# Kernel optimization log

Measured on AMD Instinct MI355X. Metric: run time of the kernel, lower is better.

## Reference

```python
import jax, jax.numpy as jnp
import numpy as np

EPS_BN = 1e-5
EPS_COS = 1e-8

N, F_IN, HID, OUT, S, NNZ = 50000, 1024, 256, 280, 5000, 800000


def setup_inputs() -> dict:
    key = jax.random.key(0)
    ks = jax.random.split(key, 20)
    inp = {}
    inp["x"] = jax.random.normal(ks[0], (N, F_IN), jnp.float32)
    inp["y"] = jax.random.normal(ks[1], (S, OUT), jnp.float32)
    inp["adj_rows"] = jax.random.randint(ks[2], (NNZ,), 0, N, jnp.int32)
    inp["adj_cols"] = jax.random.randint(ks[3], (NNZ,), 0, N, jnp.int32)
    inp["adj_vals"] = jax.random.uniform(ks[4], (NNZ,), jnp.float32)
    inp["agg_rows"] = jax.random.randint(ks[5], (N,), 0, S, jnp.int32)
    inp["agg_vals"] = jax.random.uniform(ks[6], (N,), jnp.float32)
    inp["perm"] = jax.random.permutation(ks[7], N).astype(jnp.int32)
    # parameters (kaiming-ish scale)
    def lin(k, fi, fo):
        k1, k2 = jax.random.split(k)
        w = jax.random.normal(k1, (fi, fo), jnp.float32) / np.sqrt(fi)
        b = jax.random.normal(k2, (fo,), jnp.float32) * 0.01
        return w, b
    inp["mlp_W"], inp["mlp_b"] = lin(ks[8], F_IN, HID)
    inp["bn_gamma"] = jnp.ones((HID,), jnp.float32)
    inp["bn_beta"] = jnp.zeros((HID,), jnp.float32)
    inp["hg_W1"], inp["hg_b1"] = lin(ks[9], HID, HID)
    inp["hg_W2"], inp["hg_b2"] = lin(ks[10], HID, HID)
    inp["hg_prelu"] = jnp.float32(0.25)
    inp["pred_W"], inp["pred_b"] = lin(ks[11], HID, OUT)
    inp["dgi_W"], inp["dgi_b"] = lin(ks[12], HID, OUT)
    inp["dgi_prelu"] = jnp.float32(0.25)
    return inp


def _spmm(rows, cols, vals, M, n_out):
    # sparse(H) @ M : gather source rows, scale by edge value, scatter-add to dest
    return jax.ops.segment_sum(vals[:, None] * M[cols], rows, num_segments=n_out)


def _prelu(t, a):
    return jnp.where(t >= 0, t, a * t)


def _leaky(t, s):
    return jnp.where(t >= 0, t, s * t)


def reference(x, y, adj_rows, adj_cols, adj_vals, agg_rows, agg_vals, perm,
              mlp_W, mlp_b, bn_gamma, bn_beta, hg_W1, hg_b1, hg_W2, hg_b2,
              hg_prelu, pred_W, pred_b, dgi_W, dgi_b, dgi_prelu):
    n = x.shape[0]
    s = y.shape[0]
    # mlp: Linear -> LeakyReLU(0.1) -> BatchNorm1d (batch stats, training mode)
    h0 = _leaky(x @ mlp_W + mlp_b, 0.1)
    mu = jnp.mean(h0, axis=0)
    var = jnp.mean((h0 - mu) ** 2, axis=0)  # biased, as torch BN training
    h0 = bn_gamma * (h0 - mu) * jax.lax.rsqrt(var + EPS_BN) + bn_beta
    # HGNN, num_layers=2 (dropout = identity in eval)
    t = _spmm(adj_rows, adj_cols, adj_vals, h0 @ hg_W1 + hg_b1, n)
    t = _prelu(t, hg_prelu)
    t = _spmm(adj_rows, adj_cols, adj_vals, t @ hg_W2 + hg_b2, n)
    h = _leaky(t, 0.01)
    x_prime = _leaky(h @ pred_W + pred_b, 0.01)
    # Xenium: loss = MSE(agg_mtx @ x_prime, y); agg_mtx has one nnz per cell
    agg = jax.ops.segment_sum(agg_vals[:, None] * x_prime, agg_rows, num_segments=s)
    loss = jnp.mean((agg - y) ** 2)
    # DGI (1-layer HGNN with PReLU)
    h1 = _prelu(_spmm(adj_rows, adj_cols, adj_vals, h0 @ dgi_W + dgi_b, n), dgi_prelu)
    c = jnp.mean(h1, axis=0)  # (OUT,)
    h2 = _prelu(_spmm(adj_rows, adj_cols, adj_vals, h0[perm] @ dgi_W + dgi_b, n), dgi_prelu)
    c_norm = jnp.linalg.norm(c)
    def cos(hm):
        return (hm @ c) / jnp.maximum(jnp.linalg.norm(hm, axis=1) * c_norm, EPS_COS)
    loss = loss + jnp.mean(1.0 - cos(h1)) + jnp.mean(jnp.maximum(cos(h2), 0.0))
    return (loss, x_prime)
```

## Files before the change

### kernel.cpp

```cpp
#include <hip/hip_runtime.h>
#include <hip/hip_bf16.h>

#define DEVI __device__ __forceinline__

typedef __attribute__((ext_vector_type(8))) short short8;
typedef __attribute__((ext_vector_type(4))) float float4v;

DEVI float bf2f(__hip_bfloat16 v) { return __bfloat162float(v); }
DEVI float ldbs(const ushort* p, size_t i) { return bf2f(((const __hip_bfloat16*)p)[i]); }
DEVI ushort f2bs(float v) {
    __hip_bfloat16 h = __float2bfloat16(v);
    return *(ushort*)&h;
}
DEVI float bfs2f(short s) {
    ushort u = (ushort)s;
    return bf2f(*(__hip_bfloat16*)&u);
}

DEVI float ldin(const void* p, size_t i, int isf32) {
    return isf32 ? ((const float*)p)[i] : bf2f(((const __hip_bfloat16*)p)[i]);
}
DEVI void stio(void* p, size_t i, float v, int isf32) {
    if (isf32) ((float*)p)[i] = v;
    else ((ushort*)p)[i] = f2bs(v);
}

template <int ACT>
DEVI float act_fn(float v, float alpha) {
    if (ACT == 1) return v >= 0.f ? v : 0.1f * v;
    if (ACT == 2) return v >= 0.f ? v : 0.01f * v;
    if (ACT == 3) return v >= 0.f ? v : alpha * v;
    return v;
}

DEVI float waveRed(float v) {
#pragma unroll
    for (int o = 32; o > 0; o >>= 1) v += __shfl_down(v, o);
    return v;
}

DEVI float blockRed(float v) {
    __shared__ float sm[16];
    int lane = threadIdx.x & 63, w = threadIdx.x >> 6;
    v = waveRed(v);
    if (lane == 0) sm[w] = v;
    __syncthreads();
    if (w == 0) {
        int nw = (blockDim.x + 63) >> 6;
        v = (lane < nw) ? sm[lane] : 0.f;
        v = waveRed(v);
    }
    return v;
}

__global__ void probe_k(const void* __restrict__ x, int* __restrict__ flag) {
    __shared__ int sfails;
    int t = threadIdx.x;
    if (t == 0) sfails = 0;
    __syncthreads();
    const __hip_bfloat16* xb = (const __hip_bfloat16*)x;
    int my = 0;
    for (int i = t; i < 4096; i += 256) {
        float v = bf2f(xb[i]);
        float a = fabsf(v);
        if (!(a <= 64.f) || (v != 0.f && a < 1e-6f)) my++;
    }
    atomicAdd(&sfails, my);
    __syncthreads();
    if (t == 0) flag[0] = (sfails > 409) ? 1 : 0;
}

struct Cvt5 {
    const void* src[5];
    ushort* dst[5];
    int K[5];
    int N[5];
};
__global__ void cvt_all_k(Cvt5 d, const int* __restrict__ flagp) {
    int f32 = flagp[0];
    int seg = blockIdx.y;
    int idx = blockIdx.x * blockDim.x + threadIdx.x;
    int K = d.K[seg], Nc = d.N[seg];
    int total = K * Nc;
    if (idx < total) {
        int k = idx / Nc, n = idx % Nc;
        d.dst[seg][(size_t)n * K + k] = f2bs(ldin(d.src[seg], idx, f32));
    }
}

#define TP 40
template <int AMODE, int ACT, int OMODE>
__global__ __launch_bounds__(256) void mgemm_k(
    const void* __restrict__ A, const ushort* __restrict__ Bt,
    const void* __restrict__ bias, void* __restrict__ outp, ushort* __restrict__ outp2,
    const int* __restrict__ flagp, int M, int K, int Nc, int LDo) {
    __shared__ short As[128 * TP];
    __shared__ short Bs[128 * TP];
    const int f32 = flagp[0];
    const int tid = threadIdx.x;
    const int lane = tid & 63;
    const int l15 = lane & 15;
    const int quad = lane >> 4;
    const int wid = tid >> 6;
    const int mW = (wid >> 1) * 64;
    const int nW = (wid & 1) * 64;
    const int mBase = blockIdx.y * 128;
    const int nBase = blockIdx.x * 128;

    float4v acc[4][4];
#pragma unroll
    for (int i = 0; i < 4; i++)
#pragma unroll
        for (int j = 0; j < 4; j++) acc[i][j] = (float4v){0.f, 0.f, 0.f, 0.f};

    short8 sa[2], sb[2];
    float4v fa[2][2];

    auto issue_tile = [&](int k0) {
#pragma unroll
        for (int i = 0; i < 2; i++) {
            int chunk = i * 256 + tid;
            int row = chunk >> 2;
            int c = chunk & 3;
            int gr = mBase + row;
            int gn = nBase + row;
            size_t geA = (size_t)gr * K + k0 + c * 8;
            if (AMODE == 0 && f32) {
                if (gr < M) {
                    const float* af = (const float*)A + geA;
                    fa[i][0] = *(const float4v*)af;
                    fa[i][1] = *(const float4v*)(af + 4);
                } else {
                    fa[i][0] = (float4v){0.f, 0.f, 0.f, 0.f};
                    fa[i][1] = (float4v){0.f, 0.f, 0.f, 0.f};
                }
            } else {
                sa[i] = (gr < M) ? *(const short8*)((const ushort*)A + geA)
                                 : (short8){0, 0, 0, 0, 0, 0, 0, 0};
            }
            sb[i] = (gn < Nc) ? *(const short8*)(Bt + (size_t)gn * K + k0 + c * 8)
                              : (short8){0, 0, 0, 0, 0, 0, 0, 0};
        }
    };

    auto commit_tile = [&]() {
#pragma unroll
        for (int i = 0; i < 2; i++) {
            int chunk = i * 256 + tid;
            int row = chunk >> 2;
            int c = chunk & 3;
            short8 va;
            if (AMODE == 0 && f32) {
#pragma unroll
                for (int j = 0; j < 4; j++) va[j] = (short)f2bs(fa[i][0][j]);
#pragma unroll
                for (int j = 0; j < 4; j++) va[4 + j] = (short)f2bs(fa[i][1][j]);
            } else {
                va = sa[i];
            }
            *(short8*)&As[row * TP + c * 8] = va;
            *(short8*)&Bs[row * TP + c * 8] = sb[i];
        }
    };

    const int nk = K >> 5;
    issue_tile(0);
    for (int t = 0; t < nk; ++t) {
        __syncthreads();
        commit_tile();
        if (t + 1 < nk) issue_tile((t + 1) << 5);
        __syncthreads();

        short8 af[4], bf[4];
#pragma unroll
        for (int i = 0; i < 4; i++)
            af[i] = *(const short8*)&As[(mW + i * 16 + l15) * TP + quad * 8];
#pragma unroll
        for (int j = 0; j < 4; j++)
            bf[j] = *(const short8*)&Bs[(nW + j * 16 + l15) * TP + quad * 8];
#pragma unroll
        for (int i = 0; i < 4; i++)
#pragma unroll
            for (int j = 0; j < 4; j++)
                acc[i][j] =
                    __builtin_amdgcn_mfma_f32_16x16x32_bf16(af[i], bf[j], acc[i][j], 0, 0, 0);
    }

#pragma unroll
    for (int i = 0; i < 4; i++) {
#pragma unroll
        for (int j = 0; j < 4; j++) {
            int gcn = nBase + nW + j * 16 + l15;
            if (gcn >= Nc) continue;
            float bv = ldin(bias, gcn, f32);
#pragma unroll
            for (int r = 0; r < 4; r++) {
                int grm = mBase + mW + i * 16 + quad * 4 + r;
                if (grm >= M) continue;
                float v = act_fn<ACT>(acc[i][j][r] + bv, 0.f);
                if (OMODE == 1) {
                    stio(outp, 1 + (size_t)grm * Nc + gcn, v, f32);
                    outp2[(size_t)grm * LDo + gcn] = f2bs(v);
                } else {
                    ((ushort*)outp)[(size_t)grm * LDo + gcn] = f2bs(v);
                }
            }
        }
    }
}

__global__ void count_k(const int* __restrict__ rows, int* __restrict__ counts, int nnz) {
    int i = blockIdx.x * blockDim.x + threadIdx.x;
    if (i < nnz) atomicAdd(&counts[rows[i]], 1);
}

__global__ __launch_bounds__(1024) void scan_local_k(const int* __restrict__ counts,
                                                     int* __restrict__ offs,
                                                     int* __restrict__ bsums, int n) {
    __shared__ int sm[1024];
    int t = threadIdx.x;
    int g = blockIdx.x * 1024 + t;
    int v = (g < n) ? counts[g] : 0;
    sm[t] = v;
    __syncthreads();
    for (int d = 1; d < 1024; d <<= 1) {
        int add = (t >= d) ? sm[t - d] : 0;
        __syncthreads();
        sm[t] += add;
        __syncthreads();
    }
    if (g < n) offs[g] = sm[t] - v;
    if (t == 1023) bsums[blockIdx.x] = sm[t];
}

__global__ void scan_bsums_k(int* bsums, int nb) {
    if (threadIdx.x == 0 && blockIdx.x == 0) {
        int acc = 0;
        for (int i = 0; i < nb; i++) {
            int v = bsums[i];
            bsums[i] = acc;
            acc += v;
        }
    }
}

__global__ void scan_add_k(int* __restrict__ offs, const int* __restrict__ bsums, int n, int nnz) {
    int g = blockIdx.x * blockDim.x + threadIdx.x;
    if (g < n) offs[g] += bsums[g >> 10];
    if (g == 0) offs[n] = nnz;
}

__global__ void fill_k(const int* __restrict__ rows, const int* __restrict__ cols,
                       const void* __restrict__ vals, const int* __restrict__ perm,
                       const int* __restrict__ offs, int* __restrict__ cursor,
                       int* __restrict__ cols_s, int* __restrict__ colsp_s,
                       float* __restrict__ vals_s, const int* __restrict__ flagp, int nnz) {
    int e = blockIdx.x * blockDim.x + threadIdx.x;
    if (e < nnz) {
        int r = rows[e];
        int pos = offs[r] + atomicAdd(&cursor[r], 1);
        int c = cols[e];
        cols_s[pos] = c;
        colsp_s[pos] = perm[c];
        vals_s[pos] = ldin(vals, e, flagp[0]);
    }
}

__global__ void fill_s_k(const int* __restrict__ rows, const void* __restrict__ vals,
                         const int* __restrict__ offs, int* __restrict__ cursor,
                         int* __restrict__ idx_s, float* __restrict__ val_s,
                         const int* __restrict__ flagp, int n) {
    int e = blockIdx.x * blockDim.x + threadIdx.x;
    if (e < n) {
        int r = rows[e];
        int pos = offs[r] + atomicAdd(&cursor[r], 1);
        idx_s[pos] = e;
        val_s[pos] = ldin(vals, e, flagp[0]);
    }
}

template <int ACT, bool DUAL>
__global__ __launch_bounds__(256) void spmmv_k(
    const int* __restrict__ offs, const int* __restrict__ cols_s,
    const int* __restrict__ colsp_s, const float* __restrict__ vals_s,
    const void* __restrict__ alpha_p, const int* __restrict__ flagp,
    const ushort* __restrict__ Min, ushort* __restrict__ out1, ushort* __restrict__ out2,
    int Nrow, int F, int LDin) {
    int row = blockIdx.x * 4 + (threadIdx.x >> 6);
    if (row >= Nrow) return;
    int lane = threadIdx.x & 63;
    int half = lane >> 5, l5 = lane & 31;
    int FC = F >> 3;
    bool has1 = (l5 + 32) < FC;
    float alpha = (ACT == 3) ? ldin(alpha_p, 0, flagp[0]) : 0.f;
    int s = offs[row], e = offs[row + 1];
    float a0[8] = {}, a1[8] = {}, b0[8] = {}, b1[8] = {};

    constexpr int DEPTH = DUAL ? 2 : 4;
    int i = s + half;
    for (; i + 2 * (DEPTH - 1) < e; i += 2 * DEPTH) {
        int c[DEPTH];
        float v[DEPTH];
        int cp[DEPTH];
#pragma unroll
        for (int u = 0; u < DEPTH; u++) {
            c[u] = cols_s[i + 2 * u];
            v[u] = vals_s[i + 2 * u];
        }
        if (DUAL) {
#pragma unroll
            for (int u = 0; u < DEPTH; u++) cp[u] = colsp_s[i + 2 * u];
        }
        short8 h0v[DEPTH], h1v[DEPTH], g0v[DEPTH], g1v[DEPTH];
#pragma unroll
        for (int u = 0; u < DEPTH; u++) {
            const ushort* src = Min + (size_t)c[u] * LDin;
            h0v[u] = *(const short8*)(src + l5 * 8);
            if (has1) h1v[u] = *(const short8*)(src + (l5 + 32) * 8);
            if (DUAL) {
                const ushort* srcp = Min + (size_t)cp[u] * LDin;
                g0v[u] = *(const short8*)(srcp + l5 * 8);
                if (has1) g1v[u] = *(const short8*)(srcp + (l5 + 32) * 8);
            }
        }
#pragma unroll
        for (int u = 0; u < DEPTH; u++) {
#pragma unroll
            for (int j = 0; j < 8; j++) a0[j] += v[u] * bfs2f(h0v[u][j]);
            if (has1) {
#pragma unroll
                for (int j = 0; j < 8; j++) a1[j] += v[u] * bfs2f(h1v[u][j]);
            }
            if (DUAL) {
#pragma unroll
                for (int j = 0; j < 8; j++) b0[j] += v[u] * bfs2f(g0v[u][j]);
                if (has1) {
#pragma unroll
                    for (int j = 0; j < 8; j++) b1[j] += v[u] * bfs2f(g1v[u][j]);
                }
            }
        }
    }
    for (; i < e; i += 2) {
        float v = vals_s[i];
        int c = cols_s[i];
        const ushort* src = Min + (size_t)c * LDin;
        short8 h = *(const short8*)(src + l5 * 8);
#pragma unroll
        for (int j = 0; j < 8; j++) a0[j] += v * bfs2f(h[j]);
        if (has1) {
            short8 h2 = *(const short8*)(src + (l5 + 32) * 8);
#pragma unroll
            for (int j = 0; j < 8; j++) a1[j] += v * bfs2f(h2[j]);
        }
        if (DUAL) {
            int cp = colsp_s[i];
            const ushort* srcp = Min + (size_t)cp * LDin;
            short8 g = *(const short8*)(srcp + l5 * 8);
#pragma unroll
            for (int j = 0; j < 8; j++) b0[j] += v * bfs2f(g[j]);
            if (has1) {
                short8 g2 = *(const short8*)(srcp + (l5 + 32) * 8);
#pragma unroll
                for (int j = 0; j < 8; j++) b1[j] += v * bfs2f(g2[j]);
            }
        }
    }
#pragma unroll
    for (int j = 0; j < 8; j++) {
        a0[j] += __shfl_xor(a0[j], 32);
        if (has1) a1[j] += __shfl_xor(a1[j], 32);
        if (DUAL) {
            b0[j] += __shfl_xor(b0[j], 32);
            if (has1) b1[j] += __shfl_xor(b1[j], 32);
        }
    }
    if (half == 0) {
        short8 o;
        size_t base = (size_t)row * F;
#pragma unroll
        for (int j = 0; j < 8; j++) o[j] = (short)f2bs(act_fn<ACT>(a0[j], alpha));
        *(short8*)(out1 + base + l5 * 8) = o;
        if (has1) {
#pragma unroll
            for (int j = 0; j < 8; j++) o[j] = (short)f2bs(act_fn<ACT>(a1[j], alpha));
            *(short8*)(out1 + base + (l5 + 32) * 8) = o;
        }
        if (DUAL) {
#pragma unroll
            for (int j = 0; j < 8; j++) o[j] = (short)f2bs(act_fn<ACT>(b0[j], alpha));
            *(short8*)(out2 + base + l5 * 8) = o;
            if (has1) {
#pragma unroll
                for (int j = 0; j < 8; j++) o[j] = (short)f2bs(act_fn<ACT>(b1[j], alpha));
                *(short8*)(out2 + base + (l5 + 32) * 8) = o;
            }
        }
    }
}

__global__ __launch_bounds__(256) void aggmse_k(
    const int* __restrict__ soffs, const int* __restrict__ sidx, const float* __restrict__ sval,
    const ushort* __restrict__ xp, const void* __restrict__ y, const int* __restrict__ flagp,
    float* __restrict__ lacc, int S, int F, int LDxp) {
    int srow = blockIdx.x * 4 + (threadIdx.x >> 6);
    int lane = threadIdx.x & 63;
    int half = lane >> 5, l5 = lane & 31;
    int FC = F >> 3;
    bool has1 = (l5 + 32) < FC;
    float a0[8] = {}, a1[8] = {};
    if (srow < S) {
        int s = soffs[srow], e = soffs[srow + 1];
        constexpr int DEPTH = 4;
        int i = s + half;
        for (; i + 2 * (DEPTH - 1) < e; i += 2 * DEPTH) {
            int n[DEPTH];
            float v[DEPTH];
#pragma unroll
            for (int u = 0; u < DEPTH; u++) {
                n[u] = sidx[i + 2 * u];
                v[u] = sval[i + 2 * u];
            }
            short8 h0v[DEPTH], h1v[DEPTH];
#pragma unroll
            for (int u = 0; u < DEPTH; u++) {
                const ushort* src = xp + (size_t)n[u] * LDxp;
                h0v[u] = *(const short8*)(src + l5 * 8);
                if (has1) h1v[u] = *(const short8*)(src + (l5 + 32) * 8);
            }
#pragma unroll
            for (int u = 0; u < DEPTH; u++) {
#pragma unroll
                for (int j = 0; j < 8; j++) a0[j] += v[u] * bfs2f(h0v[u][j]);
                if (has1) {
#pragma unroll
                    for (int j = 0; j < 8; j++) a1[j] += v[u] * bfs2f(h1v[u][j]);
                }
            }
        }
        for (; i < e; i += 2) {
            float v = sval[i];
            int n = sidx[i];
            const ushort* src = xp + (size_t)n * LDxp;
            short8 h = *(const short8*)(src + l5 * 8);
#pragma unroll
            for (int j = 0; j < 8; j++) a0[j] += v * bfs2f(h[j]);
            if (has1) {
                short8 h2 = *(const short8*)(src + (l5 + 32) * 8);
#pragma unroll
                for (int j = 0; j < 8; j++) a1[j] += v * bfs2f(h2[j]);
            }
        }
    }
#pragma unroll
    for (int j = 0; j < 8; j++) {
        a0[j] += __shfl_xor(a0[j], 32);
        if (has1) a1[j] += __shfl_xor(a1[j], 32);
    }
    float ss = 0.f;
    if (srow < S && half == 0) {
        int f32 = flagp[0];
        size_t base = (size_t)srow * F;
#pragma unroll
        for (int j = 0; j < 8; j++) {
            float d = a0[j] - ldin(y, base + l5 * 8 + j, f32);
            ss += d * d;
        }
        if (has1) {
#pragma unroll
            for (int j = 0; j < 8; j++) {
                float d = a1[j] - ldin(y, base + (l5 + 32) * 8 + j, f32);
                ss += d * d;
            }
        }
    }
    ss = blockRed(ss);
    if (threadIdx.x == 0) atomicAdd(&lacc[0], ss);
}

__global__ __launch_bounds__(256) void bn_stats_k(const ushort* __restrict__ h,
                                                  float* __restrict__ sum,
                                                  float* __restrict__ sumsq, int nrows, int rpb) {
    int c = threadIdx.x;
    int rs = blockIdx.x * rpb;
    int re = min(rs + rpb, nrows);
    float s = 0.f, s2 = 0.f;
    int H = blockDim.x;
    for (int r = rs; r < re; r++) {
        float v = ldbs(h, (size_t)r * H + c);
        s += v;
        s2 += v * v;
    }
    atomicAdd(&sum[c], s);
    atomicAdd(&sumsq[c], s2);
}

__global__ void bn_final_k(const float* __restrict__ sum, const float* __restrict__ sumsq,
                           const void* __restrict__ gamma, const void* __restrict__ beta,
                           float* __restrict__ scale, float* __restrict__ shift,
                           const int* __restrict__ flagp, int nrows) {
    int c = threadIdx.x;
    int f32 = flagp[0];
    float mu = sum[c] / nrows;
    float var = sumsq[c] / nrows - mu * mu;
    float sc = ldin(gamma, c, f32) * rsqrtf(var + 1e-5f);
    scale[c] = sc;
    shift[c] = ldin(beta, c, f32) - mu * sc;
}

__global__ __launch_bounds__(256) void bn_apply_k(ushort* __restrict__ h,
                                                  const float* __restrict__ scale,
                                                  const float* __restrict__ shift, int total8,
                                                  int H) {
    int idx = blockIdx.x * 256 + threadIdx.x;
    if (idx >= total8) return;
    size_t base = (size_t)idx * 8;
    int c = (int)(base % H);
    short8 v = *(short8*)(h + base);
    short8 o;
#pragma unroll
    for (int j = 0; j < 8; j++) o[j] = (short)f2bs(bfs2f(v[j]) * scale[c + j] + shift[c + j]);
    *(short8*)(h + base) = o;
}

__global__ __launch_bounds__(320) void colsum_k(const ushort* __restrict__ h,
                                                float* __restrict__ accum, int nrows, int F,
                                                int rpb) {
    int f = threadIdx.x;
    if (f >= F) return;
    int rs = blockIdx.x * rpb;
    int re = min(rs + rpb, nrows);
    float s = 0.f;
    for (int r = rs; r < re; r++) s += ldbs(h, (size_t)r * F + f);
    atomicAdd(&accum[f], s);
}

__global__ __launch_bounds__(320) void cfinal_k(const float* __restrict__ accum,
                                                float* __restrict__ c, float* __restrict__ cnorm,
                                                int N, int F) {
    int f = threadIdx.x;
    float v = 0.f;
    if (f < F) {
        v = accum[f] / N;
        c[f] = v;
    }
    float s2 = blockRed(v * v);
    if (threadIdx.x == 0) cnorm[0] = sqrtf(s2);
}

template <int MODE>
__global__ __launch_bounds__(256) void cos_k(const ushort* __restrict__ h,
                                             const float* __restrict__ c,
                                             const float* __restrict__ cnorm,
                                             float* __restrict__ acc, int N, int F) {
    int gw = (blockIdx.x * blockDim.x + threadIdx.x) >> 6;
    int lane = threadIdx.x & 63;
    int nw = (gridDim.x * blockDim.x) >> 6;
    float cn = cnorm[0];
    float s = 0.f;
    for (int row = gw; row < N; row += nw) {
        float dot = 0.f, nsq = 0.f;
        for (int f = lane; f < F; f += 64) {
            float v = ldbs(h, (size_t)row * F + f);
            dot += v * c[f];
            nsq += v * v;
        }
#pragma unroll
        for (int o = 32; o > 0; o >>= 1) {
            dot += __shfl_down(dot, o);
            nsq += __shfl_down(nsq, o);
        }
        if (lane == 0) {
            float cosv = dot / fmaxf(sqrtf(nsq) * cn, 1e-8f);
            s += (MODE == 1) ? fmaxf(cosv, 0.f) : cosv;
        }
    }
    s = blockRed(s);
    if (threadIdx.x == 0) atomicAdd(acc, s);
}

__global__ void final_k(const float* __restrict__ lacc, void* __restrict__ dout,
                        const int* __restrict__ flagp, int SOUT, int N) {
    if (threadIdx.x == 0 && blockIdx.x == 0) {
        float loss = lacc[0] / SOUT + (1.f - lacc[1] / N) + lacc[2] / N;
        stio(dout, 0, loss, flagp[0]);
    }
}

extern "C" void kernel_launch(void* const* d_in, const int* in_sizes, int n_in,
                              void* d_out, int out_size, void* d_ws, size_t ws_size,
                              hipStream_t stream) {
    const void* x = d_in[0];
    const void* y = d_in[1];
    const int* adj_rows = (const int*)d_in[2];
    const int* adj_cols = (const int*)d_in[3];
    const void* adj_vals = d_in[4];
    const int* agg_rows = (const int*)d_in[5];
    const void* agg_vals = d_in[6];
    const int* perm = (const int*)d_in[7];
    const void* mlp_W = d_in[8];
    const void* mlp_b = d_in[9];
    const void* bn_gamma = d_in[10];
    const void* bn_beta = d_in[11];
    const void* hg_W1 = d_in[12];
    const void* hg_b1 = d_in[13];
    const void* hg_W2 = d_in[14];
    const void* hg_b2 = d_in[15];
    const void* hg_prelu = d_in[16];
    const void* pred_W = d_in[17];
    const void* pred_b = d_in[18];
    const void* dgi_W = d_in[19];
    const void* dgi_b = d_in[20];
    const void* dgi_prelu = d_in[21];

    const int N = in_sizes[5];
    const int NNZ = in_sizes[2];
    const int F_IN = in_sizes[0] / N;
    const int HID = in_sizes[9];
    const int OUT = in_sizes[18];
    const int S = in_sizes[1] / OUT;

    const int LDP = (OUT + 63) & ~63;

    char* w = (char*)d_ws;
    size_t off = 0;
    auto alloc = [&](size_t b) -> char* {
        char* p = w + off;
        off += (b + 255) & ~(size_t)255;
        return p;
    };
    ushort* h0_bf = (ushort*)alloc((size_t)N * HID * 2);
    ushort* zA_bf = (ushort*)alloc((size_t)N * LDP * 2);
    ushort* zB_bf = (ushort*)alloc((size_t)N * OUT * 2);
    ushort* h2_bf = (ushort*)alloc((size_t)N * OUT * 2);
    ushort* xp_ws = zA_bf;
    ushort* mlpWt = (ushort*)alloc((size_t)HID * F_IN * 2);
    ushort* hgW1t = (ushort*)alloc((size_t)HID * HID * 2);
    ushort* hgW2t = (ushort*)alloc((size_t)HID * HID * 2);
    ushort* predWt = (ushort*)alloc((size_t)OUT * HID * 2);
    ushort* dgiWt = (ushort*)alloc((size_t)OUT * HID * 2);
    int* offs = (int*)alloc((size_t)(N + 1) * 4);
    int nbscan = (N + 1023) / 1024;
    int* bsums = (int*)alloc((size_t)nbscan * 4);
    int* cols_s = (int*)alloc((size_t)NNZ * 4);
    int* colsp_s = (int*)alloc((size_t)NNZ * 4);
    float* vals_s = (float*)alloc((size_t)NNZ * 4);
    int* soffs = (int*)alloc((size_t)(S + 1) * 4);
    int nbscan_s = (S + 1023) / 1024;
    int* sbsums = (int*)alloc((size_t)nbscan_s * 4);
    int* sidx = (int*)alloc((size_t)N * 4);
    float* sval = (float*)alloc((size_t)N * 4);
    float* bn_scale = (float*)alloc((size_t)HID * 4);
    float* bn_shift = (float*)alloc((size_t)HID * 4);
    float* c_vec = (float*)alloc((size_t)OUT * 4);
    float* cnorm = (float*)alloc(4);
    int* dflag = (int*)alloc(16);
    char* zero_base = w + off;
    int* counts = (int*)alloc((size_t)N * 4);
    int* cursor = (int*)alloc((size_t)N * 4);
    int* scnt = (int*)alloc((size_t)S * 4);
    int* scursor = (int*)alloc((size_t)S * 4);
    float* bn_sum = (float*)alloc((size_t)HID * 4);
    float* bn_sumsq = (float*)alloc((size_t)HID * 4);
    float* c_acc = (float*)alloc((size_t)OUT * 4);
    float* lacc = (float*)alloc(16);
    size_t zero_bytes = (w + off) - zero_base;
    hipMemsetAsync(zero_base, 0, zero_bytes, stream);

    probe_k<<<1, 256, 0, stream>>>(x, dflag);

    Cvt5 cv;
    cv.src[0] = mlp_W;  cv.dst[0] = mlpWt;  cv.K[0] = F_IN; cv.N[0] = HID;
    cv.src[1] = hg_W1;  cv.dst[1] = hgW1t;  cv.K[1] = HID;  cv.N[1] = HID;
    cv.src[2] = hg_W2;  cv.dst[2] = hgW2t;  cv.K[2] = HID;  cv.N[2] = HID;
    cv.src[3] = pred_W; cv.dst[3] = predWt; cv.K[3] = HID;  cv.N[3] = OUT;
    cv.src[4] = dgi_W;  cv.dst[4] = dgiWt;  cv.K[4] = HID;  cv.N[4] = OUT;
    cvt_all_k<<<dim3((F_IN * HID + 255) / 256, 5), 256, 0, stream>>>(cv, dflag);

    count_k<<<(NNZ + 255) / 256, 256, 0, stream>>>(adj_rows, counts, NNZ);
    scan_local_k<<<nbscan, 1024, 0, stream>>>(counts, offs, bsums, N);
    scan_bsums_k<<<1, 64, 0, stream>>>(bsums, nbscan);
    scan_add_k<<<(N + 255) / 256, 256, 0, stream>>>(offs, bsums, N, NNZ);
    fill_k<<<(NNZ + 255) / 256, 256, 0, stream>>>(adj_rows, adj_cols, adj_vals, perm, offs,
                                                  cursor, cols_s, colsp_s, vals_s, dflag, NNZ);
    count_k<<<(N + 255) / 256, 256, 0, stream>>>(agg_rows, scnt, N);
    scan_local_k<<<nbscan_s, 1024, 0, stream>>>(scnt, soffs, sbsums, S);
    scan_bsums_k<<<1, 64, 0, stream>>>(sbsums, nbscan_s);
    scan_add_k<<<(S + 255) / 256, 256, 0, stream>>>(soffs, sbsums, S, N);
    fill_s_k<<<(N + 255) / 256, 256, 0, stream>>>(agg_rows, agg_vals, soffs, scursor, sidx, sval,
                                                  dflag, N);

    const int MT = (N + 127) / 128;
    const int SPB = (N + 3) / 4;
    mgemm_k<0, 1, 0><<<dim3((HID + 127) / 128, MT), 256, 0, stream>>>(
        x, mlpWt, mlp_b, h0_bf, nullptr, dflag, N, F_IN, HID, HID);
    bn_stats_k<<<(N + 127) / 128, HID, 0, stream>>>(h0_bf, bn_sum, bn_sumsq, N, 128);
    bn_final_k<<<1, HID, 0, stream>>>(bn_sum, bn_sumsq, bn_gamma, bn_beta, bn_scale, bn_shift,
                                      dflag, N);
    {
        int total8 = (N * HID) / 8;
        bn_apply_k<<<(total8 + 255) / 256, 256, 0, stream>>>(h0_bf, bn_scale, bn_shift, total8,
                                                             HID);
    }

    mgemm_k<1, 0, 0><<<dim3((HID + 127) / 128, MT), 256, 0, stream>>>(
        h0_bf, hgW1t, hg_b1, zA_bf, nullptr, dflag, N, HID, HID, HID);
    spmmv_k<3, false><<<SPB, 256, 0, stream>>>(offs, cols_s, colsp_s, vals_s, hg_prelu, dflag,
                                               zA_bf, zB_bf, nullptr, N, HID, HID);
    mgemm_k<1, 0, 0><<<dim3((HID + 127) / 128, MT), 256, 0, stream>>>(
        zB_bf, hgW2t, hg_b2, zA_bf, nullptr, dflag, N, HID, HID, HID);
    spmmv_k<2, false><<<SPB, 256, 0, stream>>>(offs, cols_s, colsp_s, vals_s, nullptr, dflag,
                                               zA_bf, zB_bf, nullptr, N, HID, HID);

    mgemm_k<1, 2, 1><<<dim3((OUT + 127) / 128, MT), 256, 0, stream>>>(
        zB_bf, predWt, pred_b, d_out, xp_ws, dflag, N, HID, OUT, LDP);
    aggmse_k<<<(S + 3) / 4, 256, 0, stream>>>(soffs, sidx, sval, xp_ws, y, dflag, lacc, S, OUT,
                                              LDP);

    mgemm_k<1, 0, 0><<<dim3((OUT + 127) / 128, MT), 256, 0, stream>>>(
        h0_bf, dgiWt, dgi_b, zA_bf, nullptr, dflag, N, HID, OUT, LDP);
    spmmv_k<3, true><<<SPB, 256, 0, stream>>>(offs, cols_s, colsp_s, vals_s, dgi_prelu, dflag,
                                              zA_bf, zB_bf, h2_bf, N, OUT, LDP);
    colsum_k<<<(N + 127) / 128, 320, 0, stream>>>(zB_bf, c_acc, N, OUT, 128);
    cfinal_k<<<1, 320, 0, stream>>>(c_acc, c_vec, cnorm, N, OUT);
    cos_k<0><<<256, 256, 0, stream>>>(zB_bf, c_vec, cnorm, &lacc[1], N, OUT);
    cos_k<1><<<256, 256, 0, stream>>>(h2_bf, c_vec, cnorm, &lacc[2], N, OUT);

    final_k<<<1, 64, 0, stream>>>(lacc, d_out, dflag, S * OUT, N);
}
```

Baseline: 1.282 ms.

## Reassociate sparse aggregation before GEMMs and share aggregated h0 across branches

Uses A(XW+b) = (AX)W + rowsum(A)·b to aggregate h0 once (plus its permuted version) with a dual SpMM, then feeds the result into the HGNN layer-1 and both DGI GEMMs. Row sums of the adjacency values are accumulated in the fill kernel, and the GEMM epilogue gains a row-scaled bias and a PReLU activation. The SpMM kernel is rewritten to split the features into 8 slices of 32 columns, each handled by a separate block with 16 edges in flight per wave. This removes two SpMMs over the 280-wide features, at the cost of an extra dual GEMM pass, float atomics on the row sums, and different bf16 rounding order.

```diff
diff --git a/kernel.cpp b/kernel.cpp
--- a/kernel.cpp
+++ b/kernel.cpp
@@ -89,10 +89,11 @@
 }
 
 #define TP 40
-template <int AMODE, int ACT, int OMODE>
+template <int AMODE, int ACT, int OMODE, int BMODE>
 __global__ __launch_bounds__(256) void mgemm_k(
     const void* __restrict__ A, const ushort* __restrict__ Bt,
-    const void* __restrict__ bias, void* __restrict__ outp, ushort* __restrict__ outp2,
+    const void* __restrict__ bias, const float* __restrict__ rsc,
+    const void* __restrict__ alpha_p, void* __restrict__ outp, ushort* __restrict__ outp2,
     const int* __restrict__ flagp, int M, int K, int Nc, int LDo) {
     __shared__ short As[128 * TP];
     __shared__ short Bs[128 * TP];
@@ -186,6 +187,7 @@
                     __builtin_amdgcn_mfma_f32_16x16x32_bf16(af[i], bf[j], acc[i][j], 0, 0, 0);
     }
 
+    const float alpha = (ACT == 3) ? ldin(alpha_p, 0, f32) : 0.f;
 #pragma unroll
     for (int i = 0; i < 4; i++) {
 #pragma unroll
@@ -197,7 +199,8 @@
             for (int r = 0; r < 4; r++) {
                 int grm = mBase + mW + i * 16 + quad * 4 + r;
                 if (grm >= M) continue;
-                float v = act_fn<ACT>(acc[i][j][r] + bv, 0.f);
+                float be = (BMODE == 1) ? rsc[grm] * bv : bv;
+                float v = act_fn<ACT>(acc[i][j][r] + be, alpha);
                 if (OMODE == 1) {
                     stio(outp, 1 + (size_t)grm * Nc + gcn, v, f32);
                     outp2[(size_t)grm * LDo + gcn] = f2bs(v);
@@ -254,15 +257,18 @@
                        const void* __restrict__ vals, const int* __restrict__ perm,
                        const int* __restrict__ offs, int* __restrict__ cursor,
                        int* __restrict__ cols_s, int* __restrict__ colsp_s,
-                       float* __restrict__ vals_s, const int* __restrict__ flagp, int nnz) {
+                       float* __restrict__ vals_s, float* __restrict__ rsum,
+                       const int* __restrict__ flagp, int nnz) {
     int e = blockIdx.x * blockDim.x + threadIdx.x;
     if (e < nnz) {
         int r = rows[e];
         int pos = offs[r] + atomicAdd(&cursor[r], 1);
         int c = cols[e];
+        float v = ldin(vals, e, flagp[0]);
         cols_s[pos] = c;
         colsp_s[pos] = perm[c];
-        vals_s[pos] = ldin(vals, e, flagp[0]);
+        vals_s[pos] = v;
+        atomicAdd(&rsum[r], v);
     }
 }
 
@@ -280,121 +286,53 @@
 }
 
 template <int ACT, bool DUAL>
-__global__ __launch_bounds__(256) void spmmv_k(
+__global__ __launch_bounds__(256) void spmms_k(
     const int* __restrict__ offs, const int* __restrict__ cols_s,
     const int* __restrict__ colsp_s, const float* __restrict__ vals_s,
     const void* __restrict__ alpha_p, const int* __restrict__ flagp,
     const ushort* __restrict__ Min, ushort* __restrict__ out1, ushort* __restrict__ out2,
-    int Nrow, int F, int LDin) {
-    int row = blockIdx.x * 4 + (threadIdx.x >> 6);
+    int Nrow, int LD) {
+    int bid = blockIdx.x;
+    int slice = bid & 7;
+    int row = (bid >> 3) * 4 + (threadIdx.x >> 6);
     if (row >= Nrow) return;
     int lane = threadIdx.x & 63;
-    int half = lane >> 5, l5 = lane & 31;
-    int FC = F >> 3;
-    bool has1 = (l5 + 32) < FC;
+    int e = lane >> 2, ch = lane & 3;
+    int sbase = slice * 32 + ch * 8;
     float alpha = (ACT == 3) ? ldin(alpha_p, 0, flagp[0]) : 0.f;
-    int s = offs[row], e = offs[row + 1];
-    float a0[8] = {}, a1[8] = {}, b0[8] = {}, b1[8] = {};
-
-    constexpr int DEPTH = DUAL ? 2 : 4;
-    int i = s + half;
-    for (; i + 2 * (DEPTH - 1) < e; i += 2 * DEPTH) {
-        int c[DEPTH];
-        float v[DEPTH];
-        int cp[DEPTH];
-#pragma unroll
-        for (int u = 0; u < DEPTH; u++) {
-            c[u] = cols_s[i + 2 * u];
-            v[u] = vals_s[i + 2 * u];
-        }
-        if (DUAL) {
-#pragma unroll
-            for (int u = 0; u < DEPTH; u++) cp[u] = colsp_s[i + 2 * u];
-        }
-        short8 h0v[DEPTH], h1v[DEPTH], g0v[DEPTH], g1v[DEPTH];
-#pragma unroll
-        for (int u = 0; u < DEPTH; u++) {
-            const ushort* src = Min + (size_t)c[u] * LDin;
-            h0v[u] = *(const short8*)(src + l5 * 8);
-            if (has1) h1v[u] = *(const short8*)(src + (l5 + 32) * 8);
-            if (DUAL) {
-                const ushort* srcp = Min + (size_t)cp[u] * LDin;
-                g0v[u] = *(const short8*)(srcp + l5 * 8);
-                if (has1) g1v[u] = *(const short8*)(srcp + (l5 + 32) * 8);
-            }
-        }
-#pragma unroll
-        for (int u = 0; u < DEPTH; u++) {
-#pragma unroll
-            for (int j = 0; j < 8; j++) a0[j] += v[u] * bfs2f(h0v[u][j]);
-            if (has1) {
-#pragma unroll
-                for (int j = 0; j < 8; j++) a1[j] += v[u] * bfs2f(h1v[u][j]);
-            }
-            if (DUAL) {
-#pragma unroll
-                for (int j = 0; j < 8; j++) b0[j] += v[u] * bfs2f(g0v[u][j]);
-                if (has1) {
-#pragma unroll
-                    for (int j = 0; j < 8; j++) b1[j] += v[u] * bfs2f(g1v[u][j]);
-                }
-            }
-        }
-    }
-    for (; i < e; i += 2) {
+    int s = offs[row], en = offs[row + 1];
+    float a[8] = {}, b[8] = {};
+    for (int i = s + e; i < en; i += 16) {
+        int c = cols_s[i];
         float v = vals_s[i];
-        int c = cols_s[i];
-        const ushort* src = Min + (size_t)c * LDin;
-        short8 h = *(const short8*)(src + l5 * 8);
-#pragma unroll
-        for (int j = 0; j < 8; j++) a0[j] += v * bfs2f(h[j]);
-        if (has1) {
-            short8 h2 = *(const short8*)(src + (l5 + 32) * 8);
-#pragma unroll
-            for (int j = 0; j < 8; j++) a1[j] += v * bfs2f(h2[j]);
-        }
+        short8 h = *(const short8*)(Min + (size_t)c * LD + sbase);
+#pragma unroll
+        for (int j = 0; j < 8; j++) a[j] += v * bfs2f(h[j]);
         if (DUAL) {
             int cp = colsp_s[i];
-            const ushort* srcp = Min + (size_t)cp * LDin;
-            short8 g = *(const short8*)(srcp + l5 * 8);
-#pragma unroll
-            for (int j = 0; j < 8; j++) b0[j] += v * bfs2f(g[j]);
-            if (has1) {
-                short8 g2 = *(const short8*)(srcp + (l5 + 32) * 8);
-#pragma unroll
-                for (int j = 0; j < 8; j++) b1[j] += v * bfs2f(g2[j]);
-            }
-        }
-    }
-#pragma unroll
-    for (int j = 0; j < 8; j++) {
-        a0[j] += __shfl_xor(a0[j], 32);
-        if (has1) a1[j] += __shfl_xor(a1[j], 32);
+            short8 g = *(const short8*)(Min + (size_t)cp * LD + sbase);
+#pragma unroll
+            for (int j = 0; j < 8; j++) b[j] += v * bfs2f(g[j]);
+        }
+    }
+#pragma unroll
+    for (int m = 4; m < 64; m <<= 1) {
+#pragma unroll
+        for (int j = 0; j < 8; j++) {
+            a[j] += __shfl_xor(a[j], m);
+            if (DUAL) b[j] += __shfl_xor(b[j], m);
+        }
+    }
+    if (e == 0) {
+        short8 o;
+        size_t obase = (size_t)row * LD + sbase;
+#pragma unroll
+        for (int j = 0; j < 8; j++) o[j] = (short)f2bs(act_fn<ACT>(a[j], alpha));
+        *(short8*)(out1 + obase) = o;
         if (DUAL) {
-            b0[j] += __shfl_xor(b0[j], 32);
-            if (has1) b1[j] += __shfl_xor(b1[j], 32);
-        }
-    }
-    if (half == 0) {
-        short8 o;
-        size_t base = (size_t)row * F;
-#pragma unroll
-        for (int j = 0; j < 8; j++) o[j] = (short)f2bs(act_fn<ACT>(a0[j], alpha));
-        *(short8*)(out1 + base + l5 * 8) = o;
-        if (has1) {
-#pragma unroll
-            for (int j = 0; j < 8; j++) o[j] = (short)f2bs(act_fn<ACT>(a1[j], alpha));
-            *(short8*)(out1 + base + (l5 + 32) * 8) = o;
-        }
-        if (DUAL) {
-#pragma unroll
-            for (int j = 0; j < 8; j++) o[j] = (short)f2bs(act_fn<ACT>(b0[j], alpha));
-            *(short8*)(out2 + base + l5 * 8) = o;
-            if (has1) {
-#pragma unroll
-                for (int j = 0; j < 8; j++) o[j] = (short)f2bs(act_fn<ACT>(b1[j], alpha));
-                *(short8*)(out2 + base + (l5 + 32) * 8) = o;
-            }
+#pragma unroll
+            for (int j = 0; j < 8; j++) o[j] = (short)f2bs(act_fn<ACT>(b[j], alpha));
+            *(short8*)(out2 + obase) = o;
         }
     }
 }
@@ -630,8 +568,10 @@
         return p;
     };
     ushort* h0_bf = (ushort*)alloc((size_t)N * HID * 2);
+    ushort* U_bf = (ushort*)alloc((size_t)N * HID * 2);
+    ushort* Up_bf = (ushort*)alloc((size_t)N * HID * 2);
     ushort* zA_bf = (ushort*)alloc((size_t)N * LDP * 2);
-    ushort* zB_bf = (ushort*)alloc((size_t)N * OUT * 2);
+    ushort* zB_bf = (ushort*)alloc((size_t)N * LDP * 2);
     ushort* h2_bf = (ushort*)alloc((size_t)N * OUT * 2);
     ushort* xp_ws = zA_bf;
     ushort* mlpWt = (ushort*)alloc((size_t)HID * F_IN * 2);
@@ -660,6 +600,7 @@
     int* cursor = (int*)alloc((size_t)N * 4);
     int* scnt = (int*)alloc((size_t)S * 4);
     int* scursor = (int*)alloc((size_t)S * 4);
+    float* rsum = (float*)alloc((size_t)N * 4);
     float* bn_sum = (float*)alloc((size_t)HID * 4);
     float* bn_sumsq = (float*)alloc((size_t)HID * 4);
     float* c_acc = (float*)alloc((size_t)OUT * 4);
@@ -682,7 +623,8 @@
     scan_bsums_k<<<1, 64, 0, stream>>>(bsums, nbscan);
     scan_add_k<<<(N + 255) / 256, 256, 0, stream>>>(offs, bsums, N, NNZ);
     fill_k<<<(NNZ + 255) / 256, 256, 0, stream>>>(adj_rows, adj_cols, adj_vals, perm, offs,
-                                                  cursor, cols_s, colsp_s, vals_s, dflag, NNZ);
+                                                  cursor, cols_s, colsp_s, vals_s, rsum, dflag,
+                                                  NNZ);
     count_k<<<(N + 255) / 256, 256, 0, stream>>>(agg_rows, scnt, N);
     scan_local_k<<<nbscan_s, 1024, 0, stream>>>(scnt, soffs, sbsums, S);
     scan_bsums_k<<<1, 64, 0, stream>>>(sbsums, nbscan_s);
@@ -691,9 +633,12 @@
                                                   dflag, N);
 
     const int MT = (N + 127) / 128;
-    const int SPB = (N + 3) / 4;
-    mgemm_k<0, 1, 0><<<dim3((HID + 127) / 128, MT), 256, 0, stream>>>(
-        x, mlpWt, mlp_b, h0_bf, nullptr, dflag, N, F_IN, HID, HID);
+    const int NT_H = (HID + 127) / 128;
+    const int NT_O = (OUT + 127) / 128;
+    const int SGRID = ((N + 3) / 4) * 8;
+
+    mgemm_k<0, 1, 0, 0><<<dim3(NT_H, MT), 256, 0, stream>>>(
+        x, mlpWt, mlp_b, nullptr, nullptr, h0_bf, nullptr, dflag, N, F_IN, HID, HID);
     bn_stats_k<<<(N + 127) / 128, HID, 0, stream>>>(h0_bf, bn_sum, bn_sumsq, N, 128);
     bn_final_k<<<1, HID, 0, stream>>>(bn_sum, bn_sumsq, bn_gamma, bn_beta, bn_scale, bn_shift,
                                       dflag, N);
@@ -703,24 +648,26 @@
                                                              HID);
     }
 
-    mgemm_k<1, 0, 0><<<dim3((HID + 127) / 128, MT), 256, 0, stream>>>(
-        h0_bf, hgW1t, hg_b1, zA_bf, nullptr, dflag, N, HID, HID, HID);
-    spmmv_k<3, false><<<SPB, 256, 0, stream>>>(offs, cols_s, colsp_s, vals_s, hg_prelu, dflag,
-                                               zA_bf, zB_bf, nullptr, N, HID, HID);
-    mgemm_k<1, 0, 0><<<dim3((HID + 127) / 128, MT), 256, 0, stream>>>(
-        zB_bf, hgW2t, hg_b2, zA_bf, nullptr, dflag, N, HID, HID, HID);
-    spmmv_k<2, false><<<SPB, 256, 0, stream>>>(offs, cols_s, colsp_s, vals_s, nullptr, dflag,
-                                               zA_bf, zB_bf, nullptr, N, HID, HID);
-
-    mgemm_k<1, 2, 1><<<dim3((OUT + 127) / 128, MT), 256, 0, stream>>>(
-        zB_bf, predWt, pred_b, d_out, xp_ws, dflag, N, HID, OUT, LDP);
+    spmms_k<0, true><<<SGRID, 256, 0, stream>>>(offs, cols_s, colsp_s, vals_s, nullptr, dflag,
+                                                h0_bf, U_bf, Up_bf, N, HID);
+
+    mgemm_k<1, 3, 0, 1><<<dim3(NT_H, MT), 256, 0, stream>>>(
+        U_bf, hgW1t, hg_b1, rsum, hg_prelu, zB_bf, nullptr, dflag, N, HID, HID, HID);
+    mgemm_k<1, 0, 0, 0><<<dim3(NT_H, MT), 256, 0, stream>>>(
+        zB_bf, hgW2t, hg_b2, nullptr, nullptr, zA_bf, nullptr, dflag, N, HID, HID, HID);
+    spmms_k<2, false><<<SGRID, 256, 0, stream>>>(offs, cols_s, nullptr, vals_s, nullptr, dflag,
+                                                 zA_bf, zB_bf, nullptr, N, HID);
+
+    mgemm_k<1, 2, 1, 0><<<dim3(NT_O, MT), 256, 0, stream>>>(
+        zB_bf, predWt, pred_b, nullptr, nullptr, d_out, xp_ws, dflag, N, HID, OUT, LDP);
     aggmse_k<<<(S + 3) / 4, 256, 0, stream>>>(soffs, sidx, sval, xp_ws, y, dflag, lacc, S, OUT,
                                               LDP);
 
-    mgemm_k<1, 0, 0><<<dim3((OUT + 127) / 128, MT), 256, 0, stream>>>(
-        h0_bf, dgiWt, dgi_b, zA_bf, nullptr, dflag, N, HID, OUT, LDP);
-    spmmv_k<3, true><<<SPB, 256, 0, stream>>>(offs, cols_s, colsp_s, vals_s, dgi_prelu, dflag,
-                                              zA_bf, zB_bf, h2_bf, N, OUT, LDP);
+    mgemm_k<1, 3, 0, 1><<<dim3(NT_O, MT), 256, 0, stream>>>(
+        U_bf, dgiWt, dgi_b, rsum, dgi_prelu, zB_bf, nullptr, dflag, N, HID, OUT, OUT);
+    mgemm_k<1, 3, 0, 1><<<dim3(NT_O, MT), 256, 0, stream>>>(
+        Up_bf, dgiWt, dgi_b, rsum, dgi_prelu, h2_bf, nullptr, dflag, N, HID, OUT, OUT);
+
     colsum_k<<<(N + 127) / 128, 320, 0, stream>>>(zB_bf, c_acc, N, OUT, 128);
     cfinal_k<<<1, 320, 0, stream>>>(c_acc, c_vec, cnorm, N, OUT);
     cos_k<0><<<256, 256, 0, stream>>>(zB_bf, c_vec, cnorm, &lacc[1], N, OUT);
```

After: 1.488 ms. +16.0%, slower.
